# Kernel tuning notes

Measured on AMD Instinct MI355X. Metric: run time of the kernel, lower is better.

## Reference

```python
import jax, jax.numpy as jnp
import numpy as np

B, T, NIN, H, L = 64, 256, 512, 1024, 2


def _lstm_layer(x, h0, c0, w_ih, w_hh, b_ih, b_hh):
    # x: [B, T, in]; precompute input projections for all timesteps
    xw = jnp.einsum('bti,gi->btg', x, w_ih) + b_ih + b_hh  # [B, T, 4H]

    def step(carry, xt):
        h, c = carry
        gates = xt + h @ w_hh.T  # [B, 4H]
        i, f, g, o = jnp.split(gates, 4, axis=-1)  # torch gate order i,f,g,o
        i = jax.nn.sigmoid(i)
        f = jax.nn.sigmoid(f)
        g = jnp.tanh(g)
        o = jax.nn.sigmoid(o)
        c = f * c + i * g
        h = o * jnp.tanh(c)
        return (h, c), h

    (hT, cT), hs = jax.lax.scan(step, (h0, c0), jnp.swapaxes(xw, 0, 1))
    return jnp.swapaxes(hs, 0, 1), hT, cT  # [B,T,H], [B,H], [B,H]


def setup_inputs() -> dict:
    key = jax.random.key(0)
    ks = jax.random.split(key, 16)
    s = 1.0 / np.sqrt(H)
    u = lambda k, shp: jax.random.uniform(k, shp, jnp.float32, -s, s)
    inp = {
        'x': jax.random.normal(ks[0], (B, T, NIN), jnp.float32),
        'h0': jnp.zeros((L, B, H), jnp.float32),
        'c0': jnp.zeros((L, B, H), jnp.float32),
        'w_ih_0': u(ks[1], (4 * H, NIN)),
        'w_hh_0': u(ks[2], (4 * H, H)),
        'b_ih_0': u(ks[3], (4 * H,)),
        'b_hh_0': u(ks[4], (4 * H,)),
        'w_ih_1': u(ks[5], (4 * H, H)),
        'w_hh_1': u(ks[6], (4 * H, H)),
        'b_ih_1': u(ks[7], (4 * H,)),
        'b_hh_1': u(ks[8], (4 * H,)),
        'w_dec': jax.random.uniform(ks[9], (NIN, H), jnp.float32, -0.1, 0.1),
        'b_dec': jnp.zeros((NIN,), jnp.float32),
    }
    return inp


def reference(x, h0, c0, w_ih_0, w_hh_0, b_ih_0, b_hh_0,
              w_ih_1, w_hh_1, b_ih_1, b_hh_1, w_dec, b_dec):
    out0, h0n, c0n = _lstm_layer(x, h0[0], c0[0], w_ih_0, w_hh_0, b_ih_0, b_hh_0)
    out1, h1n, c1n = _lstm_layer(out0, h0[1], c0[1], w_ih_1, w_hh_1, b_ih_1, b_hh_1)
    # eval mode: dropout layers inactive (train_mode=False)
    decoded = out1[:, -1, :] @ w_dec.T + b_dec  # [B, NIN]
    logp = jax.nn.log_softmax(decoded, axis=1)
    hn = jnp.stack([h0n, h1n], axis=0)
    cn = jnp.stack([c0n, c1n], axis=0)
    return logp, hn, cn
```

## Files before the change

### kernel.cpp

```cpp
#include <hip/hip_runtime.h>

#define BATCH   64
#define TSTEPS  256
#define NINPUT  512
#define HDIM    1024
#define G4      4096
#define NSCAN   64
#define NHC     16
#define NGEMM   128

typedef __attribute__((ext_vector_type(8))) short short8;
typedef __attribute__((ext_vector_type(4))) float f32x4;
typedef __attribute__((ext_vector_type(4))) unsigned int u32x4;
typedef __attribute__((ext_vector_type(2))) unsigned int u32x2;

static __device__ __forceinline__ unsigned short f2bf(float x) {
    unsigned u = __float_as_uint(x);
    unsigned r = 0x7fffu + ((u >> 16) & 1u);
    return (unsigned short)((u + r) >> 16);
}
static __device__ __forceinline__ float bf2f(unsigned short b) {
    return __uint_as_float(((unsigned)b) << 16);
}
static __device__ __forceinline__ float sigf(float x) {
    return 1.f / (1.f + __expf(-x));
}
static __device__ __forceinline__ float tanhf_fast(float x) {
    return 2.f / (1.f + __expf(-2.f * x)) - 1.f;
}

__global__ void k_poison(u32x4* __restrict__ p, long n4) {
    long i = (long)blockIdx.x * blockDim.x + threadIdx.x;
    long st = (long)gridDim.x * blockDim.x;
    u32x4 v = (u32x4){0xFFFFFFFFu, 0xFFFFFFFFu, 0xFFFFFFFFu, 0xFFFFFFFFu};
    for (; i < n4; i += st) p[i] = v;
}

__global__ void k_f2b(const float* __restrict__ in, unsigned short* __restrict__ out, long n) {
    long i = (long)blockIdx.x * blockDim.x + threadIdx.x;
    long stride = (long)gridDim.x * blockDim.x;
    for (long j = i * 4; j < n; j += stride * 4) {
        float4 v = *reinterpret_cast<const float4*>(in + j);
        ushort4 o;
        o.x = f2bf(v.x); o.y = f2bf(v.y); o.z = f2bf(v.z); o.w = f2bf(v.w);
        *reinterpret_cast<ushort4*>(out + j) = o;
    }
}

__global__ void k_f2b_tm(const float* __restrict__ in, unsigned short* __restrict__ out) {
    const long total = (long)BATCH * TSTEPS * NINPUT;
    long v = ((long)blockIdx.x * blockDim.x + threadIdx.x) * 4;
    const long stride = (long)gridDim.x * blockDim.x * 4;
    for (; v < total; v += stride) {
        long row = v / NINPUT;
        int i = (int)(v - row * NINPUT);
        int b = (int)(row / TSTEPS);
        int t = (int)(row - (long)b * TSTEPS);
        float4 f = *reinterpret_cast<const float4*>(in + v);
        ushort4 o;
        o.x = f2bf(f.x); o.y = f2bf(f.y); o.z = f2bf(f.z); o.w = f2bf(f.w);
        *reinterpret_cast<ushort4*>(out + ((size_t)t * BATCH + b) * NINPUT + i) = o;
    }
}

__global__ void k_prep_small(const float* __restrict__ bih0, const float* __restrict__ bhh0,
                             const float* __restrict__ bih1, const float* __restrict__ bhh1,
                             float* __restrict__ bb0, float* __restrict__ bb1,
                             const float* __restrict__ h0,
                             unsigned short* __restrict__ hA0, unsigned short* __restrict__ hA1) {
    int i = blockIdx.x * blockDim.x + threadIdx.x;
    if (i < G4) { bb0[i] = bih0[i] + bhh0[i]; bb1[i] = bih1[i] + bhh1[i]; }
    if (i < BATCH * HDIM) {
        hA0[i] = f2bf(h0[i]);
        hA1[i] = f2bf(h0[BATCH * HDIM + i]);
    }
}

#define BM 128
#define BN 128
#define BK 64

static __device__ __forceinline__ void g2l16(const unsigned short* g, void* lds) {
    __builtin_amdgcn_global_load_lds(
        (const __attribute__((address_space(1))) unsigned int*)g,
        (__attribute__((address_space(3))) unsigned int*)lds, 16, 0, 0);
}

__global__ __launch_bounds__(256)
void k_gemm_bt(const unsigned short* __restrict__ A,
               const unsigned short* __restrict__ B,
               const float* __restrict__ bias,
               unsigned short* __restrict__ C,
               int M, int N, int K)
{
    __shared__ unsigned short As[BM * BK];
    __shared__ unsigned short Bs[BN * BK];
    const int tid = threadIdx.x;
    const int lane = tid & 63, wv = tid >> 6;
    const int nbn = N / BN;
    const int bm0 = (blockIdx.x / nbn) * BM;
    const int bn0 = (blockIdx.x % nbn) * BN;
    const int wr = wv >> 1, wc = wv & 1;

    f32x4 acc[4][4];
#pragma unroll
    for (int i = 0; i < 4; i++)
#pragma unroll
        for (int j = 0; j < 4; j++) acc[i][j] = (f32x4){0.f, 0.f, 0.f, 0.f};

    const int srow = tid >> 3;
    const int scb  = (tid & 7) * 16;

    for (int kt = 0; kt < K; kt += BK) {
        __syncthreads();
#pragma unroll
        for (int is = 0; is < 4; is++) {
            int row = is * 32 + srow;
            int kb = scb ^ ((row & 7) << 4);
            g2l16(A + (size_t)(bm0 + row) * K + kt + (kb >> 1),
                  (char*)As + is * 4096 + wv * 1024);
        }
#pragma unroll
        for (int is = 0; is < 4; is++) {
            int row = is * 32 + srow;
            int kb = scb ^ ((row & 7) << 4);
            g2l16(B + (size_t)(bn0 + row) * K + kt + (kb >> 1),
                  (char*)Bs + is * 4096 + wv * 1024);
        }
        asm volatile("s_waitcnt vmcnt(0)" ::: "memory");
        __syncthreads();

#pragma unroll
        for (int ks = 0; ks < 2; ks++) {
            short8 a[4], b[4];
            const int kb = ks * 64 + ((lane >> 4) << 4);
#pragma unroll
            for (int mt = 0; mt < 4; mt++) {
                int r = wr * 64 + mt * 16 + (lane & 15);
                a[mt] = *reinterpret_cast<const short8*>(
                    (const char*)As + r * 128 + (kb ^ ((r & 7) << 4)));
            }
#pragma unroll
            for (int nt = 0; nt < 4; nt++) {
                int n = wc * 64 + nt * 16 + (lane & 15);
                b[nt] = *reinterpret_cast<const short8*>(
                    (const char*)Bs + n * 128 + (kb ^ ((n & 7) << 4)));
            }
#pragma unroll
            for (int mt = 0; mt < 4; mt++)
#pragma unroll
                for (int nt = 0; nt < 4; nt++)
                    acc[mt][nt] = __builtin_amdgcn_mfma_f32_16x16x32_bf16(
                        a[mt], b[nt], acc[mt][nt], 0, 0, 0);
        }
    }

#pragma unroll
    for (int nt = 0; nt < 4; nt++) {
        int cg = bn0 + wc * 64 + nt * 16 + (lane & 15);
        float bv = bias[cg];
#pragma unroll
        for (int mt = 0; mt < 4; mt++) {
#pragma unroll
            for (int e = 0; e < 4; e++) {
                int rg = bm0 + wr * 64 + mt * 16 + ((lane >> 4) << 2) + e;
                C[(size_t)rg * N + cg] = f2bf(acc[mt][nt][e] + bv);
            }
        }
    }
}


template<int L>
static __device__ void scan_body(const unsigned short* __restrict__ whh,
                                 const unsigned short* __restrict__ xw,
                                 const float* __restrict__ c0,
                                 const unsigned short* __restrict__ h0b,
                                 unsigned short* __restrict__ ring,
                                 float* __restrict__ hn, float* __restrict__ cn,
                                 const unsigned* __restrict__ gflags,
                                 unsigned* __restrict__ hflags,
                                 int wg, char* smem)
{
    float (*plds)[64][34] = reinterpret_cast<float (*)[64][34]>(smem);
    const int tid = threadIdx.x;
    const int lane = tid & 63, kw = tid >> 6;
    const int colbase = wg * NHC;

    short8 bfr[4][8];
    {
        const int c = lane & 15;
#pragma unroll
        for (int g = 0; g < 4; g++) {
            int grow = g * HDIM + colbase + c;
#pragma unroll
            for (int s = 0; s < 8; s++) {
                int k = kw * 256 + s * 32 + ((lane >> 4) << 3);
                bfr[g][s] = *reinterpret_cast<const short8*>(whh + (size_t)grow * HDIM + k);
            }
        }
    }

    const int r2 = tid >> 2;
    const int u0 = (tid & 3) * 4;
    f32x4 cst = *reinterpret_cast<const f32x4*>(c0 + (size_t)r2 * HDIM + colbase + u0);

    const int arow = lane & 15;
    const size_t koff = (size_t)kw * 256 + ((lane >> 4) << 3);

    for (int t = 0; t < TSTEPS; t++) {
        const unsigned short* xp = xw + ((size_t)t * BATCH + r2) * G4 + colbase + u0;
        u32x2 xi, xf, xg, xo;
        if (L == 0) {
            xi = *reinterpret_cast<const u32x2*>(xp);
            xf = *reinterpret_cast<const u32x2*>(xp + HDIM);
            xg = *reinterpret_cast<const u32x2*>(xp + 2 * HDIM);
            xo = *reinterpret_cast<const u32x2*>(xp + 3 * HDIM);
        } else {
            const unsigned* gf = gflags + (size_t)(t >> 1) * 32 + (colbase >> 7);
            for (;;) {
                unsigned a, b, c, d;
                asm volatile("global_load_dword %0, %1, off sc0 sc1" : "=v"(a) : "v"(gf));
                asm volatile("global_load_dword %0, %1, off sc0 sc1" : "=v"(b) : "v"(gf + 8));
                asm volatile("global_load_dword %0, %1, off sc0 sc1" : "=v"(c) : "v"(gf + 16));
                asm volatile("global_load_dword %0, %1, off sc0 sc1" : "=v"(d) : "v"(gf + 24));
                asm volatile("s_waitcnt vmcnt(0)" ::: "memory");
                __builtin_amdgcn_sched_barrier(0);
                if ((a & b & c & d) != 0) break;
                __builtin_amdgcn_s_sleep(1);
            }
            asm volatile("global_load_dwordx2 %0, %1, off sc0 sc1" : "=v"(xi) : "v"(xp));
            asm volatile("global_load_dwordx2 %0, %1, off sc0 sc1" : "=v"(xf) : "v"(xp + HDIM));
            asm volatile("global_load_dwordx2 %0, %1, off sc0 sc1" : "=v"(xg) : "v"(xp + 2 * HDIM));
            asm volatile("global_load_dwordx2 %0, %1, off sc0 sc1" : "=v"(xo) : "v"(xp + 3 * HDIM));
        }

        const unsigned short* pa0;
        if (t == 0)       pa0 = h0b + (size_t)arow * HDIM + koff;
        else if (L == 0)  pa0 = ring + ((size_t)(t - 1) * BATCH + arow) * HDIM + koff;
        else              pa0 = ring + ((size_t)((t - 1) & 3) * BATCH + arow) * HDIM + koff;
        const unsigned short* pa1 = pa0 + 16 * HDIM;
        const unsigned short* pa2 = pa0 + 32 * HDIM;
        const unsigned short* pa3 = pa0 + 48 * HDIM;

        u32x4 afr[8][4];
#define ISSUE4(S, OFFS) \
        asm volatile("global_load_dwordx4 %0, %1, off offset:" OFFS " sc0 sc1" : "=v"(afr[S][0]) : "v"(pa0)); \
        asm volatile("global_load_dwordx4 %0, %1, off offset:" OFFS " sc0 sc1" : "=v"(afr[S][1]) : "v"(pa1)); \
        asm volatile("global_load_dwordx4 %0, %1, off offset:" OFFS " sc0 sc1" : "=v"(afr[S][2]) : "v"(pa2)); \
        asm volatile("global_load_dwordx4 %0, %1, off offset:" OFFS " sc0 sc1" : "=v"(afr[S][3]) : "v"(pa3));

        if (L == 0) {
            for (;;) {
                ISSUE4(0, "0")   ISSUE4(1, "64")  ISSUE4(2, "128") ISSUE4(3, "192")
                ISSUE4(4, "256") ISSUE4(5, "320") ISSUE4(6, "384") ISSUE4(7, "448")
                asm volatile("s_waitcnt vmcnt(0)" ::: "memory");
                __builtin_amdgcn_sched_barrier(0);
                unsigned mx = 0;
#pragma unroll
                for (int s = 0; s < 8; s++)
#pragma unroll
                    for (int m = 0; m < 4; m++) {
                        u32x4 u = afr[s][m];
                        unsigned a = u[0] > u[1] ? u[0] : u[1];
                        unsigned b = u[2] > u[3] ? u[2] : u[3];
                        unsigned c = a > b ? a : b;
                        mx = mx > c ? mx : c;
                    }
                if (!__any(mx >= 0xFFFF0000u)) break;
                __builtin_amdgcn_s_sleep(1);
            }
        } else {
            if (t > 0) {
                const unsigned* fp = hflags + (size_t)(t - 1) * 64 + lane;
                for (;;) {
                    unsigned v;
                    asm volatile("global_load_dword %0, %1, off sc0 sc1" : "=v"(v) : "v"(fp));
                    asm volatile("s_waitcnt vmcnt(0)" ::: "memory");
                    __builtin_amdgcn_sched_barrier(0);
                    if (__all(v != 0)) break;
                    __builtin_amdgcn_s_sleep(1);
                }
            }
            ISSUE4(0, "0")   ISSUE4(1, "64")  ISSUE4(2, "128") ISSUE4(3, "192")
            ISSUE4(4, "256") ISSUE4(5, "320") ISSUE4(6, "384") ISSUE4(7, "448")
            asm volatile("s_waitcnt vmcnt(0)" ::: "memory");
            __builtin_amdgcn_sched_barrier(0);
        }
#undef ISSUE4

        f32x4 acc[4][4];
#pragma unroll
        for (int m = 0; m < 4; m++)
#pragma unroll
            for (int g = 0; g < 4; g++) acc[m][g] = (f32x4){0.f, 0.f, 0.f, 0.f};
#pragma unroll
        for (int s = 0; s < 8; s++)
#pragma unroll
            for (int m = 0; m < 4; m++) {
                short8 av = __builtin_bit_cast(short8, afr[s][m]);
#pragma unroll
                for (int g = 0; g < 4; g++)
                    acc[m][g] = __builtin_amdgcn_mfma_f32_16x16x32_bf16(
                        av, bfr[g][s], acc[m][g], 0, 0, 0);
            }

#pragma unroll
        for (int m = 0; m < 4; m++)
#pragma unroll
            for (int g = 0; g < 2; g++) {
                int col = g * 16 + (lane & 15);
                int rb = m * 16 + ((lane >> 4) << 2);
#pragma unroll
                for (int e = 0; e < 4; e++)
                    plds[kw][rb + e][col] = acc[m][g][e];
            }
        __syncthreads();
        f32x4 sI = (f32x4){0.f,0.f,0.f,0.f}, sF = sI;
#pragma unroll
        for (int w = 0; w < 4; w++) {
            sI += *reinterpret_cast<const f32x4*>(&plds[w][r2][u0]);
            sF += *reinterpret_cast<const f32x4*>(&plds[w][r2][16 + u0]);
        }
        __syncthreads();
#pragma unroll
        for (int m = 0; m < 4; m++)
#pragma unroll
            for (int g = 2; g < 4; g++) {
                int col = (g - 2) * 16 + (lane & 15);
                int rb = m * 16 + ((lane >> 4) << 2);
#pragma unroll
                for (int e = 0; e < 4; e++)
                    plds[kw][rb + e][col] = acc[m][g][e];
            }
        __syncthreads();
        f32x4 sG = (f32x4){0.f,0.f,0.f,0.f}, sO = sG;
#pragma unroll
        for (int w = 0; w < 4; w++) {
            sG += *reinterpret_cast<const f32x4*>(&plds[w][r2][u0]);
            sO += *reinterpret_cast<const f32x4*>(&plds[w][r2][16 + u0]);
        }
        __syncthreads();

#define ADDX(S, V) { unsigned lo = V[0], hi = V[1]; \
        S[0] += bf2f((unsigned short)lo); S[1] += bf2f((unsigned short)(lo >> 16)); \
        S[2] += bf2f((unsigned short)hi); S[3] += bf2f((unsigned short)(hi >> 16)); }
        ADDX(sI, xi) ADDX(sF, xf) ADDX(sG, xg) ADDX(sO, xo)
#undef ADDX

        float hv[4];
#pragma unroll
        for (int j = 0; j < 4; j++) {
            float c = sigf(sF[j]) * cst[j] + sigf(sI[j]) * tanhf_fast(sG[j]);
            cst[j] = c;
            hv[j] = sigf(sO[j]) * tanhf_fast(c);
        }
        u32x2 hp;
        hp[0] = (unsigned)f2bf(hv[0]) | ((unsigned)f2bf(hv[1]) << 16);
        hp[1] = (unsigned)f2bf(hv[2]) | ((unsigned)f2bf(hv[3]) << 16);
        unsigned short* wp;
        if (L == 0) wp = ring + ((size_t)t * BATCH + r2) * HDIM + colbase + u0;
        else        wp = ring + ((size_t)(t & 3) * BATCH + r2) * HDIM + colbase + u0;
        asm volatile("global_store_dwordx2 %0, %1, off sc0 sc1"
                     :: "v"(wp), "v"(hp) : "memory");

        if (t == TSTEPS - 1) {
            const size_t hi_ = (size_t)r2 * HDIM + colbase + u0;
            *reinterpret_cast<f32x4*>(hn + hi_) = (f32x4){hv[0], hv[1], hv[2], hv[3]};
            *reinterpret_cast<f32x4*>(cn + hi_) = cst;
        }

        if (L == 1) {
            asm volatile("s_waitcnt vmcnt(0)" ::: "memory");
            __syncthreads();
            if (tid == 0) {
                unsigned one = 1;
                asm volatile("global_store_dword %0, %1, off sc0 sc1"
                             :: "v"(hflags + (size_t)t * 64 + wg), "v"(one) : "memory");
            }
        }
    }
}

static __device__ void gemm_body(const unsigned short* __restrict__ A,
                                 const unsigned short* __restrict__ B,
                                 const float* __restrict__ bias,
                                 unsigned short* __restrict__ C,
                                 unsigned* __restrict__ gflags,
                                 int gw, char* smem)
{
    unsigned short* As = reinterpret_cast<unsigned short*>(smem);
    unsigned short* Bs = As + BM * BK;
    const int tid = threadIdx.x;
    const int lane = tid & 63, wv = tid >> 6;
    const int wr = wv >> 1, wc = wv & 1;
    const int srow = tid >> 3;
    const int scb  = (tid & 7) * 16;

    for (int i = 0; i < 32; i++) {
        const int j = i * NGEMM + gw;
        const int mt = j >> 5;
        const int nt = j & 31;
        const int bm0 = mt * BM, bn0 = nt * BN;

        {
            const unsigned short* lr = A + ((size_t)bm0 + 127) * HDIM + lane * 16;
            for (;;) {
                unsigned v;
                asm volatile("global_load_dword %0, %1, off sc0 sc1" : "=v"(v) : "v"(lr));
                asm volatile("s_waitcnt vmcnt(0)" ::: "memory");
                __builtin_amdgcn_sched_barrier(0);
                if (!__any(v >= 0xFFFF0000u)) break;
                __builtin_amdgcn_s_sleep(16);
            }
        }

        f32x4 acc[4][4];
#pragma unroll
        for (int a = 0; a < 4; a++)
#pragma unroll
            for (int b = 0; b < 4; b++) acc[a][b] = (f32x4){0.f, 0.f, 0.f, 0.f};

        for (int kt = 0; kt < HDIM; kt += BK) {
            __syncthreads();
#pragma unroll
            for (int is = 0; is < 4; is++) {
                int row = is * 32 + srow;
                int kb = scb ^ ((row & 7) << 4);
                g2l16(B + (size_t)(bn0 + row) * HDIM + kt + (kb >> 1),
                      (char*)Bs + is * 4096 + wv * 1024);
            }
            const unsigned short* ap[4];
#pragma unroll
            for (int is = 0; is < 4; is++) {
                int row = is * 32 + srow;
                int kb = scb ^ ((row & 7) << 4);
                ap[is] = A + (size_t)(bm0 + row) * HDIM + kt + (kb >> 1);
            }
            u32x4 av0, av1, av2, av3;
            for (;;) {
                asm volatile("global_load_dwordx4 %0, %1, off sc0 sc1" : "=v"(av0) : "v"(ap[0]));
                asm volatile("global_load_dwordx4 %0, %1, off sc0 sc1" : "=v"(av1) : "v"(ap[1]));
                asm volatile("global_load_dwordx4 %0, %1, off sc0 sc1" : "=v"(av2) : "v"(ap[2]));
                asm volatile("global_load_dwordx4 %0, %1, off sc0 sc1" : "=v"(av3) : "v"(ap[3]));
                asm volatile("s_waitcnt vmcnt(0)" ::: "memory");
                __builtin_amdgcn_sched_barrier(0);
                unsigned mx = 0;
#pragma unroll
                for (int e = 0; e < 4; e++) {
                    unsigned a01 = av0[e] > av1[e] ? av0[e] : av1[e];
                    unsigned a23 = av2[e] > av3[e] ? av2[e] : av3[e];
                    unsigned m = a01 > a23 ? a01 : a23;
                    mx = mx > m ? mx : m;
                }
                if (mx < 0xFFFF0000u) break;
                __builtin_amdgcn_s_sleep(2);
            }
            char* asb = (char*)As;
            *reinterpret_cast<u32x4*>(asb + 0 * 4096 + wv * 1024 + lane * 16) = av0;
            *reinterpret_cast<u32x4*>(asb + 1 * 4096 + wv * 1024 + lane * 16) = av1;
            *reinterpret_cast<u32x4*>(asb + 2 * 4096 + wv * 1024 + lane * 16) = av2;
            *reinterpret_cast<u32x4*>(asb + 3 * 4096 + wv * 1024 + lane * 16) = av3;
            __syncthreads();

#pragma unroll
            for (int ks = 0; ks < 2; ks++) {
                short8 a[4], b[4];
                const int kb = ks * 64 + ((lane >> 4) << 4);
#pragma unroll
                for (int m = 0; m < 4; m++) {
                    int r = wr * 64 + m * 16 + (lane & 15);
                    a[m] = *reinterpret_cast<const short8*>(
                        (const char*)As + r * 128 + (kb ^ ((r & 7) << 4)));
                }
#pragma unroll
                for (int n = 0; n < 4; n++) {
                    int nn = wc * 64 + n * 16 + (lane & 15);
                    b[n] = *reinterpret_cast<const short8*>(
                        (const char*)Bs + nn * 128 + (kb ^ ((nn & 7) << 4)));
                }
#pragma unroll
                for (int m = 0; m < 4; m++)
#pragma unroll
                    for (int n = 0; n < 4; n++)
                        acc[m][n] = __builtin_amdgcn_mfma_f32_16x16x32_bf16(
                            a[m], b[n], acc[m][n], 0, 0, 0);
            }
        }

#pragma unroll
        for (int n = 0; n < 4; n++) {
            int cg = bn0 + wc * 64 + n * 16 + (lane & 15);
            float bv = bias[cg];
#pragma unroll
            for (int m = 0; m < 4; m++) {
#pragma unroll
                for (int e = 0; e < 4; e++) {
                    int rg = bm0 + wr * 64 + m * 16 + ((lane >> 4) << 2) + e;
                    unsigned val = f2bf(acc[m][n][e] + bv);
                    const unsigned short* cp = C + (size_t)rg * G4 + cg;
                    asm volatile("global_store_short %0, %1, off sc0 sc1"
                                 :: "v"(cp), "v"(val) : "memory");
                }
            }
        }
        asm volatile("s_waitcnt vmcnt(0)" ::: "memory");
        __syncthreads();
        if (tid == 0) {
            unsigned one = 1;
            asm volatile("global_store_dword %0, %1, off sc0 sc1"
                         :: "v"(gflags + mt * 32 + nt), "v"(one) : "memory");
        }
    }
}

__global__ __launch_bounds__(256, 1)
void k_fused(const unsigned short* __restrict__ w0hb,
             const unsigned short* __restrict__ w1hb,
             const unsigned short* __restrict__ w1ib,
             const float* __restrict__ bb1,
             unsigned short* __restrict__ xw,
             unsigned short* __restrict__ ring0,
             unsigned short* __restrict__ ring1,
             const float* __restrict__ c0,
             const unsigned short* __restrict__ hA0,
             const unsigned short* __restrict__ hA1,
             float* __restrict__ hn, float* __restrict__ cn,
             unsigned* __restrict__ gflags, unsigned* __restrict__ hflags)
{
    __shared__ alignas(16) char smem[4 * 64 * 34 * 4];
    const int bid = blockIdx.x;
    if (bid < NSCAN) {
        scan_body<0>(w0hb, xw, c0, hA0, ring0, hn, cn, nullptr, nullptr, bid, smem);
    } else if (bid < NSCAN + NGEMM) {
        gemm_body(ring0, w1ib, bb1, xw, gflags, bid - NSCAN, smem);
    } else {
        scan_body<1>(w1hb, xw, c0 + BATCH * HDIM, hA1, ring1,
                     hn + BATCH * HDIM, cn + BATCH * HDIM,
                     gflags, hflags, bid - NSCAN - NGEMM, smem);
    }
}

__global__ __launch_bounds__(256)
void k_decode(const float* __restrict__ h1,
              const float* __restrict__ wdec,
              const float* __restrict__ bdec,
              float* __restrict__ out)
{
    __shared__ float hs[HDIM];
    __shared__ float ls[NINPUT];
    __shared__ float red[256];
    const int r = blockIdx.x, tid = threadIdx.x;
    reinterpret_cast<float4*>(hs)[tid] = reinterpret_cast<const float4*>(h1 + (size_t)r * HDIM)[tid];
    __syncthreads();
#pragma unroll
    for (int rep = 0; rep < 2; rep++) {
        int n = tid + rep * 256;
        float s = bdec[n];
        const float4* w4 = reinterpret_cast<const float4*>(wdec + (size_t)n * HDIM);
        for (int k = 0; k < HDIM / 4; k++) {
            float4 w = w4[k];
            float4 h4 = reinterpret_cast<const float4*>(hs)[k];
            s += w.x * h4.x + w.y * h4.y + w.z * h4.z + w.w * h4.w;
        }
        ls[n] = s;
    }
    __syncthreads();
    red[tid] = fmaxf(ls[tid], ls[tid + 256]);
    __syncthreads();
    for (int s2 = 128; s2 > 0; s2 >>= 1) {
        if (tid < s2) red[tid] = fmaxf(red[tid], red[tid + s2]);
        __syncthreads();
    }
    float M = red[0];
    __syncthreads();
    red[tid] = __expf(ls[tid] - M) + __expf(ls[tid + 256] - M);
    __syncthreads();
    for (int s2 = 128; s2 > 0; s2 >>= 1) {
        if (tid < s2) red[tid] += red[tid + s2];
        __syncthreads();
    }
    float lse = M + __logf(red[0]);
    out[(size_t)r * NINPUT + tid] = ls[tid] - lse;
    out[(size_t)r * NINPUT + tid + 256] = ls[tid + 256] - lse;
}

extern "C" void kernel_launch(void* const* d_in, const int* in_sizes, int n_in,
                              void* d_out, int out_size, void* d_ws, size_t ws_size,
                              hipStream_t stream)
{
    const float* x    = (const float*)d_in[0];
    const float* h0   = (const float*)d_in[1];
    const float* c0   = (const float*)d_in[2];
    const float* wih0 = (const float*)d_in[3];
    const float* whh0 = (const float*)d_in[4];
    const float* bih0 = (const float*)d_in[5];
    const float* bhh0 = (const float*)d_in[6];
    const float* wih1 = (const float*)d_in[7];
    const float* whh1 = (const float*)d_in[8];
    const float* bih1 = (const float*)d_in[9];
    const float* bhh1 = (const float*)d_in[10];
    const float* wdec = (const float*)d_in[11];
    const float* bdec = (const float*)d_in[12];
    float* out = (float*)d_out;

    char* ws = (char*)d_ws;
    size_t off = 0;
    auto alloc = [&](size_t bytes) -> void* {
        void* p = ws + off;
        off += (bytes + 255) & ~(size_t)255;
        return p;
    };
    unsigned short* xw    = (unsigned short*)alloc((size_t)BATCH * TSTEPS * G4 * 2);
    unsigned short* ring0 = (unsigned short*)alloc((size_t)TSTEPS * BATCH * HDIM * 2);
    unsigned short* ring1 = (unsigned short*)alloc((size_t)4 * BATCH * HDIM * 2);
    unsigned short* xb    = (unsigned short*)alloc((size_t)TSTEPS * BATCH * NINPUT * 2);
    unsigned short* w0ib  = (unsigned short*)alloc((size_t)G4 * NINPUT * 2);
    unsigned short* w0hb  = (unsigned short*)alloc((size_t)G4 * HDIM * 2);
    unsigned short* w1ib  = (unsigned short*)alloc((size_t)G4 * HDIM * 2);
    unsigned short* w1hb  = (unsigned short*)alloc((size_t)G4 * HDIM * 2);
    float*          bb0   = (float*)alloc(G4 * 4);
    float*          bb1   = (float*)alloc(G4 * 4);
    unsigned short* hA0   = (unsigned short*)alloc(BATCH * HDIM * 2);
    unsigned short* hA1   = (unsigned short*)alloc(BATCH * HDIM * 2);
    unsigned*       gflags = (unsigned*)alloc(128 * 32 * 4);
    unsigned*       hflags = (unsigned*)alloc(TSTEPS * 64 * 4);

    const long ring_n4 = (long)TSTEPS * BATCH * HDIM * 2 / 16;

    k_poison<<<2048, 256, 0, stream>>>((u32x4*)ring0, ring_n4);
    hipMemsetAsync(gflags, 0, 128 * 32 * 4 + TSTEPS * 64 * 4, stream);

    k_f2b_tm<<<1024, 256, 0, stream>>>(x, xb);
    k_f2b<<<512, 256, 0, stream>>>(wih0, w0ib, (long)G4 * NINPUT);
    k_f2b<<<1024, 256, 0, stream>>>(whh0, w0hb, (long)G4 * HDIM);
    k_f2b<<<1024, 256, 0, stream>>>(wih1, w1ib, (long)G4 * HDIM);
    k_f2b<<<1024, 256, 0, stream>>>(whh1, w1hb, (long)G4 * HDIM);
    k_prep_small<<<512, 256, 0, stream>>>(bih0, bhh0, bih1, bhh1, bb0, bb1, h0, hA0, hA1);

    const int M = BATCH * TSTEPS;
    k_gemm_bt<<<(M / BM) * (G4 / BN), 256, 0, stream>>>(xb, w0ib, bb0, xw, M, G4, NINPUT);

    k_fused<<<NSCAN + NGEMM + NSCAN, 256, 0, stream>>>(
        w0hb, w1hb, w1ib, bb1, xw, ring0, ring1, c0, hA0, hA1,
        out + 32768,
        out + 32768 + 2 * BATCH * HDIM,
        gflags, hflags);

    k_decode<<<BATCH, 256, 0, stream>>>(out + 32768 + BATCH * HDIM, wdec, bdec, out);
}
```

Baseline: 2.755 ms.

## Replace layer-1 per-step hflag barrier with poison-polling on full-length ring

Layer-1 scan now writes its hidden states to a full T-length ring, which reuses the xb/w0ib workspace and is poisoned before the fused kernel. It polls the data for the poison pattern, as layer 0 already does, instead of waiting on per-workgroup hflags written after a __syncthreads. The gflags wait is also batched: one wave-wide load checks 16 upcoming GEMM tiles and advances a watermark, so most steps skip polling. This drops a block barrier and a flag round-trip per step, at the cost of an extra poison kernel and more memory traffic for ring1.

```diff
diff --git a/kernel.cpp b/kernel.cpp
--- a/kernel.cpp
+++ b/kernel.cpp
@@ -179,13 +179,13 @@
                                  unsigned short* __restrict__ ring,
                                  float* __restrict__ hn, float* __restrict__ cn,
                                  const unsigned* __restrict__ gflags,
-                                 unsigned* __restrict__ hflags,
                                  int wg, char* smem)
 {
     float (*plds)[64][34] = reinterpret_cast<float (*)[64][34]>(smem);
     const int tid = threadIdx.x;
     const int lane = tid & 63, kw = tid >> 6;
     const int colbase = wg * NHC;
+    const int cb = wg >> 3;
 
     short8 bfr[4][8];
     {
@@ -207,6 +207,7 @@
 
     const int arow = lane & 15;
     const size_t koff = (size_t)kw * 256 + ((lane >> 4) << 3);
+    int wm = 0;
 
     for (int t = 0; t < TSTEPS; t++) {
         const unsigned short* xp = xw + ((size_t)t * BATCH + r2) * G4 + colbase + u0;
@@ -217,17 +218,19 @@
             xg = *reinterpret_cast<const u32x2*>(xp + 2 * HDIM);
             xo = *reinterpret_cast<const u32x2*>(xp + 3 * HDIM);
         } else {
-            const unsigned* gf = gflags + (size_t)(t >> 1) * 32 + (colbase >> 7);
-            for (;;) {
-                unsigned a, b, c, d;
-                asm volatile("global_load_dword %0, %1, off sc0 sc1" : "=v"(a) : "v"(gf));
-                asm volatile("global_load_dword %0, %1, off sc0 sc1" : "=v"(b) : "v"(gf + 8));
-                asm volatile("global_load_dword %0, %1, off sc0 sc1" : "=v"(c) : "v"(gf + 16));
-                asm volatile("global_load_dword %0, %1, off sc0 sc1" : "=v"(d) : "v"(gf + 24));
+            const int mt = t >> 1;
+            while (mt >= wm) {
+                int mti = wm + (lane >> 2); if (mti > 127) mti = 127;
+                const unsigned* fp = gflags + mti * 32 + (lane & 3) * 8 + cb;
+                unsigned v;
+                asm volatile("global_load_dword %0, %1, off sc0 sc1" : "=v"(v) : "v"(fp));
                 asm volatile("s_waitcnt vmcnt(0)" ::: "memory");
                 __builtin_amdgcn_sched_barrier(0);
-                if ((a & b & c & d) != 0) break;
-                __builtin_amdgcn_s_sleep(1);
+                unsigned long long mk = __ballot(v != 0);
+                int adv = 0;
+                while (adv < 16 && ((mk >> (4 * adv)) & 0xFull) == 0xFull) adv++;
+                wm += adv;
+                if (adv == 0) __builtin_amdgcn_s_sleep(8);
             }
             asm volatile("global_load_dwordx2 %0, %1, off sc0 sc1" : "=v"(xi) : "v"(xp));
             asm volatile("global_load_dwordx2 %0, %1, off sc0 sc1" : "=v"(xf) : "v"(xp + HDIM));
@@ -236,9 +239,8 @@
         }
 
         const unsigned short* pa0;
-        if (t == 0)       pa0 = h0b + (size_t)arow * HDIM + koff;
-        else if (L == 0)  pa0 = ring + ((size_t)(t - 1) * BATCH + arow) * HDIM + koff;
-        else              pa0 = ring + ((size_t)((t - 1) & 3) * BATCH + arow) * HDIM + koff;
+        if (t == 0) pa0 = h0b + (size_t)arow * HDIM + koff;
+        else        pa0 = ring + ((size_t)(t - 1) * BATCH + arow) * HDIM + koff;
         const unsigned short* pa1 = pa0 + 16 * HDIM;
         const unsigned short* pa2 = pa0 + 32 * HDIM;
         const unsigned short* pa3 = pa0 + 48 * HDIM;
@@ -249,43 +251,24 @@
         asm volatile("global_load_dwordx4 %0, %1, off offset:" OFFS " sc0 sc1" : "=v"(afr[S][1]) : "v"(pa1)); \
         asm volatile("global_load_dwordx4 %0, %1, off offset:" OFFS " sc0 sc1" : "=v"(afr[S][2]) : "v"(pa2)); \
         asm volatile("global_load_dwordx4 %0, %1, off offset:" OFFS " sc0 sc1" : "=v"(afr[S][3]) : "v"(pa3));
-
-        if (L == 0) {
-            for (;;) {
-                ISSUE4(0, "0")   ISSUE4(1, "64")  ISSUE4(2, "128") ISSUE4(3, "192")
-                ISSUE4(4, "256") ISSUE4(5, "320") ISSUE4(6, "384") ISSUE4(7, "448")
-                asm volatile("s_waitcnt vmcnt(0)" ::: "memory");
-                __builtin_amdgcn_sched_barrier(0);
-                unsigned mx = 0;
-#pragma unroll
-                for (int s = 0; s < 8; s++)
-#pragma unroll
-                    for (int m = 0; m < 4; m++) {
-                        u32x4 u = afr[s][m];
-                        unsigned a = u[0] > u[1] ? u[0] : u[1];
-                        unsigned b = u[2] > u[3] ? u[2] : u[3];
-                        unsigned c = a > b ? a : b;
-                        mx = mx > c ? mx : c;
-                    }
-                if (!__any(mx >= 0xFFFF0000u)) break;
-                __builtin_amdgcn_s_sleep(1);
-            }
-        } else {
-            if (t > 0) {
-                const unsigned* fp = hflags + (size_t)(t - 1) * 64 + lane;
-                for (;;) {
-                    unsigned v;
-                    asm volatile("global_load_dword %0, %1, off sc0 sc1" : "=v"(v) : "v"(fp));
-                    asm volatile("s_waitcnt vmcnt(0)" ::: "memory");
-                    __builtin_amdgcn_sched_barrier(0);
-                    if (__all(v != 0)) break;
-                    __builtin_amdgcn_s_sleep(1);
-                }
-            }
+        for (;;) {
             ISSUE4(0, "0")   ISSUE4(1, "64")  ISSUE4(2, "128") ISSUE4(3, "192")
             ISSUE4(4, "256") ISSUE4(5, "320") ISSUE4(6, "384") ISSUE4(7, "448")
             asm volatile("s_waitcnt vmcnt(0)" ::: "memory");
             __builtin_amdgcn_sched_barrier(0);
+            unsigned mx = 0;
+#pragma unroll
+            for (int s = 0; s < 8; s++)
+#pragma unroll
+                for (int m = 0; m < 4; m++) {
+                    u32x4 u = afr[s][m];
+                    unsigned a = u[0] > u[1] ? u[0] : u[1];
+                    unsigned b = u[2] > u[3] ? u[2] : u[3];
+                    unsigned c = a > b ? a : b;
+                    mx = mx > c ? mx : c;
+                }
+            if (!__any(mx >= 0xFFFF0000u)) break;
+            __builtin_amdgcn_s_sleep(1);
         }
 #undef ISSUE4
 
@@ -358,9 +341,7 @@
         u32x2 hp;
         hp[0] = (unsigned)f2bf(hv[0]) | ((unsigned)f2bf(hv[1]) << 16);
         hp[1] = (unsigned)f2bf(hv[2]) | ((unsigned)f2bf(hv[3]) << 16);
-        unsigned short* wp;
-        if (L == 0) wp = ring + ((size_t)t * BATCH + r2) * HDIM + colbase + u0;
-        else        wp = ring + ((size_t)(t & 3) * BATCH + r2) * HDIM + colbase + u0;
+        unsigned short* wp = ring + ((size_t)t * BATCH + r2) * HDIM + colbase + u0;
         asm volatile("global_store_dwordx2 %0, %1, off sc0 sc1"
                      :: "v"(wp), "v"(hp) : "memory");
 
@@ -368,16 +349,6 @@
             const size_t hi_ = (size_t)r2 * HDIM + colbase + u0;
             *reinterpret_cast<f32x4*>(hn + hi_) = (f32x4){hv[0], hv[1], hv[2], hv[3]};
             *reinterpret_cast<f32x4*>(cn + hi_) = cst;
-        }
-
-        if (L == 1) {
-            asm volatile("s_waitcnt vmcnt(0)" ::: "memory");
-            __syncthreads();
-            if (tid == 0) {
-                unsigned one = 1;
-                asm volatile("global_store_dword %0, %1, off sc0 sc1"
-                             :: "v"(hflags + (size_t)t * 64 + wg), "v"(one) : "memory");
-            }
         }
     }
 }
@@ -526,18 +497,18 @@
              const unsigned short* __restrict__ hA0,
              const unsigned short* __restrict__ hA1,
              float* __restrict__ hn, float* __restrict__ cn,
-             unsigned* __restrict__ gflags, unsigned* __restrict__ hflags)
+             unsigned* __restrict__ gflags)
 {
     __shared__ alignas(16) char smem[4 * 64 * 34 * 4];
     const int bid = blockIdx.x;
     if (bid < NSCAN) {
-        scan_body<0>(w0hb, xw, c0, hA0, ring0, hn, cn, nullptr, nullptr, bid, smem);
+        scan_body<0>(w0hb, xw, c0, hA0, ring0, hn, cn, nullptr, bid, smem);
     } else if (bid < NSCAN + NGEMM) {
         gemm_body(ring0, w1ib, bb1, xw, gflags, bid - NSCAN, smem);
     } else {
         scan_body<1>(w1hb, xw, c0 + BATCH * HDIM, hA1, ring1,
                      hn + BATCH * HDIM, cn + BATCH * HDIM,
-                     gflags, hflags, bid - NSCAN - NGEMM, smem);
+                     gflags, bid - NSCAN - NGEMM, smem);
     }
 }
 
@@ -611,11 +582,10 @@
         off += (bytes + 255) & ~(size_t)255;
         return p;
     };
+    const size_t ring_bytes = (size_t)TSTEPS * BATCH * HDIM * 2;
+
     unsigned short* xw    = (unsigned short*)alloc((size_t)BATCH * TSTEPS * G4 * 2);
-    unsigned short* ring0 = (unsigned short*)alloc((size_t)TSTEPS * BATCH * HDIM * 2);
-    unsigned short* ring1 = (unsigned short*)alloc((size_t)4 * BATCH * HDIM * 2);
-    unsigned short* xb    = (unsigned short*)alloc((size_t)TSTEPS * BATCH * NINPUT * 2);
-    unsigned short* w0ib  = (unsigned short*)alloc((size_t)G4 * NINPUT * 2);
+    unsigned short* ring0 = (unsigned short*)alloc(ring_bytes);
     unsigned short* w0hb  = (unsigned short*)alloc((size_t)G4 * HDIM * 2);
     unsigned short* w1ib  = (unsigned short*)alloc((size_t)G4 * HDIM * 2);
     unsigned short* w1hb  = (unsigned short*)alloc((size_t)G4 * HDIM * 2);
@@ -624,12 +594,18 @@
     unsigned short* hA0   = (unsigned short*)alloc(BATCH * HDIM * 2);
     unsigned short* hA1   = (unsigned short*)alloc(BATCH * HDIM * 2);
     unsigned*       gflags = (unsigned*)alloc(128 * 32 * 4);
-    unsigned*       hflags = (unsigned*)alloc(TSTEPS * 64 * 4);
-
-    const long ring_n4 = (long)TSTEPS * BATCH * HDIM * 2 / 16;
+    unsigned short* xb    = (unsigned short*)alloc((size_t)TSTEPS * BATCH * NINPUT * 2);
+    unsigned short* w0ib  = (unsigned short*)alloc((size_t)G4 * NINPUT * 2);
+    unsigned short* ring1 = xb;
+    {
+        size_t have = (size_t)TSTEPS * BATCH * NINPUT * 2 + (size_t)G4 * NINPUT * 2;
+        if (ring_bytes > have) alloc(ring_bytes - have);
+    }
+
+    const long ring_n4 = (long)ring_bytes / 16;
 
     k_poison<<<2048, 256, 0, stream>>>((u32x4*)ring0, ring_n4);
-    hipMemsetAsync(gflags, 0, 128 * 32 * 4 + TSTEPS * 64 * 4, stream);
+    hipMemsetAsync(gflags, 0, 128 * 32 * 4, stream);
 
     k_f2b_tm<<<1024, 256, 0, stream>>>(x, xb);
     k_f2b<<<512, 256, 0, stream>>>(wih0, w0ib, (long)G4 * NINPUT);
@@ -641,11 +617,13 @@
     const int M = BATCH * TSTEPS;
     k_gemm_bt<<<(M / BM) * (G4 / BN), 256, 0, stream>>>(xb, w0ib, bb0, xw, M, G4, NINPUT);
 
+    k_poison<<<2048, 256, 0, stream>>>((u32x4*)ring1, ring_n4);
+
     k_fused<<<NSCAN + NGEMM + NSCAN, 256, 0, stream>>>(
         w0hb, w1hb, w1ib, bb1, xw, ring0, ring1, c0, hA0, hA1,
         out + 32768,
         out + 32768 + 2 * BATCH * HDIM,
-        gflags, hflags);
+        gflags);
 
     k_decode<<<BATCH, 256, 0, stream>>>(out + 32768 + BATCH * HDIM, wdec, bdec, out);
 }
```

New measurement: 2.775 ms. About the same (+0.7%).
